# Performance work log

Hardware: AMD Instinct MI355X
Metric: run time of the kernel (lower is better)

## Reference

```python
import jax, jax.numpy as jnp
import numpy as np

D_IN = 4096
D_OUT = 4096
TOKENS = 8192


def setup_inputs() -> dict:
    key = jax.random.key(0)
    k_x, k_w = jax.random.split(key)
    x = jax.random.normal(k_x, (TOKENS, D_IN), dtype=jnp.float32)
    # int8 weight buffer (stored as int32 for jax friendliness; values in [-128,127))
    weight_i8 = jax.random.randint(k_w, (D_OUT, D_IN), -128, 127, dtype=jnp.int32)
    return {
        "x": x,
        "weight_i8": weight_i8,
        "weight_scale": jnp.array([0.01], dtype=jnp.float32),
        "weight_zero_point": jnp.zeros((1,), dtype=jnp.int32),
        "bias": jnp.zeros((D_OUT,), dtype=jnp.float32),
        "output_scale": jnp.array([0.5], dtype=jnp.float32),
        "output_zero_point": jnp.full((1,), 128, dtype=jnp.int32),
    }


def reference(x, weight_i8, weight_scale, weight_zero_point, bias,
              output_scale, output_zero_point):
    # NOTE: the torch module also computes torch.quantize_per_tensor(x, ...)
    # whose result is unused (dead code); it does not affect the output and
    # is omitted here.
    # Dequantize int8 weight: (w_int - zp) * scale  -> [D_OUT, D_IN] fp32
    w = (weight_i8.astype(jnp.float32)
         - weight_zero_point.astype(jnp.float32)) * weight_scale
    # Standard fp32 linear: [T, D_IN] @ [D_IN, D_OUT] + bias
    out = jnp.einsum("ti,oi->to", x, w) + bias
    # quantize_per_tensor(out, output_scale, output_zp, quint8).dequantize():
    # q = clamp(round(out/scale) + zp, 0, 255); deq = (q - zp) * scale
    zp = output_zero_point.astype(jnp.float32)
    q = jnp.clip(jnp.round(out / output_scale) + zp, 0.0, 255.0)
    return (q - zp) * output_scale
```

## Files before the change

kernel.cpp:

```cpp
#include <hip/hip_runtime.h>

#define TOKENS 8192
#define D_IN   4096
#define D_OUT  4096

typedef _Float16 f16;
typedef __attribute__((ext_vector_type(8))) _Float16 half8;
typedef __attribute__((ext_vector_type(4))) float    f32x4;
typedef __attribute__((address_space(3))) char       lds_char;


__global__ void cvt_x_kernel(const float* __restrict__ x, f16* __restrict__ xh) {
    size_t i = ((size_t)blockIdx.x * blockDim.x + threadIdx.x) * 4;
    float4 v = *reinterpret_cast<const float4*>(x + i);
    union { f16 h[4]; uint2 u; } p;
    p.h[0] = (f16)v.x; p.h[1] = (f16)v.y; p.h[2] = (f16)v.z; p.h[3] = (f16)v.w;
    *reinterpret_cast<uint2*>(xh + i) = p.u;
}

__global__ void cvt_w_kernel(const int* __restrict__ w, f16* __restrict__ wh,
                             const float* __restrict__ scale_p,
                             const int* __restrict__ zp_p) {
    size_t i = ((size_t)blockIdx.x * blockDim.x + threadIdx.x) * 4;
    float s = scale_p[0];
    float z = (float)zp_p[0];
    int4 v = *reinterpret_cast<const int4*>(w + i);
    union { f16 h[4]; uint2 u; } p;
    p.h[0] = (f16)(((float)v.x - z) * s);
    p.h[1] = (f16)(((float)v.y - z) * s);
    p.h[2] = (f16)(((float)v.z - z) * s);
    p.h[3] = (f16)(((float)v.w - z) * s);
    *reinterpret_cast<uint2*>(wh + i) = p.u;
}


#define BM 256
#define BN 256
#define BK 64
#define NT (D_IN / BK)
#define LDS_BUF   65536
#define LDS_B_OFF 32768

__device__ __forceinline__ void stage16(const f16* g, lds_char* l) {
    __builtin_amdgcn_global_load_lds(
        (const __attribute__((address_space(1))) void*)g,
        (__attribute__((address_space(3))) void*)l, 16, 0, 0);
}

#define LDS_LOAD8(p) (*(const __attribute__((address_space(3))) half8*)(p))

#define LOAD_A(QM)                                                          \
    do { _Pragma("unroll")                                                  \
        for (int fm = 0; fm < 4; ++fm) {                                    \
            int rr = wr * 128 + (QM) * 64 + fm * 16 + lr;                   \
            _Pragma("unroll")                                               \
            for (int ks = 0; ks < 2; ++ks)                                  \
                a[fm][ks] = LDS_LOAD8(bufA + rr * 128 +                     \
                                      ((cb0 + ks * 64) ^ swzr));            \
        } } while (0)

#define LOAD_B(QN, BV)                                                     \
    do { _Pragma("unroll")                                                  \
        for (int fn = 0; fn < 2; ++fn) {                                    \
            int rr = wc * 64 + (QN) * 32 + fn * 16 + lr;                    \
            _Pragma("unroll")                                               \
            for (int ks = 0; ks < 2; ++ks)                                  \
                BV[fn][ks] = LDS_LOAD8(bufB + rr * 128 +                    \
                                       ((cb0 + ks * 64) ^ swzr));           \
        } } while (0)

#define MFMA_QUAD(QM, QN, BV)                                               \
    do { _Pragma("unroll")                                                  \
        for (int fm = 0; fm < 4; ++fm) {                                    \
            _Pragma("unroll")                                               \
            for (int fn = 0; fn < 2; ++fn) {                                \
                _Pragma("unroll")                                           \
                for (int ks = 0; ks < 2; ++ks)                              \
                    acc[(QM)*4+fm][(QN)*2+fn] =                             \
                        __builtin_amdgcn_mfma_f32_16x16x32_f16(             \
                            a[fm][ks], BV[fn][ks],                          \
                            acc[(QM)*4+fm][(QN)*2+fn], 0, 0, 0);            \
            }                                                               \
        } } while (0)

#define FENCE()    asm volatile("" ::: "memory")
#define BAR()      __builtin_amdgcn_s_barrier()
#define VMCNT(N)   asm volatile("s_waitcnt vmcnt(" #N ")" ::: "memory")
#define PRIO(x)    __builtin_amdgcn_s_setprio(x)

__global__ __launch_bounds__(512, 2)
void gemm8p(const f16* __restrict__ A, const f16* __restrict__ B,
            const float* __restrict__ bias,
            const float* __restrict__ oscale_p, const int* __restrict__ ozp_p,
            float* __restrict__ C)
{
    __shared__ __align__(1024) char smem_[2 * LDS_BUF];
    lds_char* smem = (lds_char*)smem_;
    constexpr int K = D_IN, N = D_OUT;

    int nwg = gridDim.x;
    int cpx = nwg >> 3;
    int bid = blockIdx.x;
    int swz = (bid & 7) * cpx + (bid >> 3);
    int ntn = N / BN;
    int m0 = (swz / ntn) * BM;
    int n0 = (swz % ntn) * BN;

    int tid = threadIdx.x;
    int l   = tid & 63;
    int wv  = tid >> 6;
    int wr  = wv >> 2;
    int wc  = wv & 3;

    int srow = wv * 8 + (l >> 3);
    int scol = ((l & 7) ^ (l >> 3)) * 8;
    const f16* gA = A + (size_t)(m0 + srow) * K + scol;
    const f16* gB = B + (size_t)(n0 + srow) * K + scol;
    lds_char* dstbase = smem + wv * 1024 + l * 16;

    int lr   = l & 15;
    int swzr = (l & 7) << 4;
    int cb0  = (l >> 4) * 16;

    f32x4 acc[8][4] = {};

    #pragma unroll
    for (int q = 0; q < 4; ++q) stage16(gA + (size_t)q * 64 * K, dstbase + q * 8192);
    #pragma unroll
    for (int q = 0; q < 4; ++q) stage16(gB + (size_t)q * 64 * K, dstbase + LDS_B_OFF + q * 8192);
    VMCNT(0);
    BAR();

    half8 a[4][2], b0v[2][2], b1v[2][2];

    for (int t = 0; t < NT - 1; ++t) {
        const lds_char* bufA = smem + (t & 1) * LDS_BUF;
        const lds_char* bufB = bufA + LDS_B_OFF;
        lds_char* dst = dstbase + ((t + 1) & 1) * LDS_BUF;
        const f16* nA = gA + (size_t)(t + 1) * BK;
        const f16* nB = gB + (size_t)(t + 1) * BK;

        LOAD_A(0);
        LOAD_B(0, b0v);
        stage16(nB,                      dst + LDS_B_OFF);
        stage16(nB + (size_t)64 * K,     dst + LDS_B_OFF + 8192);
        BAR();
        PRIO(1); MFMA_QUAD(0, 0, b0v); PRIO(0);

        LOAD_B(1, b1v);
        stage16(nB + (size_t)128 * K,    dst + LDS_B_OFF + 2 * 8192);
        stage16(nB + (size_t)192 * K,    dst + LDS_B_OFF + 3 * 8192);
        BAR();
        PRIO(1); MFMA_QUAD(0, 1, b1v); PRIO(0);

        VMCNT(4);
        BAR();
        LOAD_A(1);
        stage16(nA,                      dst);
        stage16(nA + (size_t)128 * K,    dst + 2 * 8192);
        BAR();
        PRIO(1); MFMA_QUAD(1, 1, b1v); PRIO(0);

        FENCE();
        stage16(nA + (size_t)64 * K,     dst + 8192);
        stage16(nA + (size_t)192 * K,    dst + 3 * 8192);
        BAR();
        PRIO(1); MFMA_QUAD(1, 0, b0v); PRIO(0);

        VMCNT(2);
        BAR();
    }

    {
        const int t = NT - 1;
        const lds_char* bufA = smem + (t & 1) * LDS_BUF;
        const lds_char* bufB = bufA + LDS_B_OFF;

        VMCNT(0);
        BAR();

        LOAD_A(0);
        LOAD_B(0, b0v);
        LOAD_B(1, b1v);
        PRIO(1);
        MFMA_QUAD(0, 0, b0v);
        MFMA_QUAD(0, 1, b1v);
        PRIO(0);
        LOAD_A(1);
        PRIO(1);
        MFMA_QUAD(1, 1, b1v);
        MFMA_QUAD(1, 0, b0v);
        PRIO(0);
    }

    float os  = oscale_p[0];
    float ozp = (float)ozp_p[0];
    float inv = 1.0f / os;
    #pragma unroll
    for (int qm = 0; qm < 2; ++qm) {
        #pragma unroll
        for (int fm = 0; fm < 4; ++fm) {
            int rowb = m0 + wr * 128 + qm * 64 + fm * 16 + (l >> 4) * 4;
            #pragma unroll
            for (int qn = 0; qn < 2; ++qn) {
                #pragma unroll
                for (int fn = 0; fn < 2; ++fn) {
                    int col = n0 + wc * 64 + qn * 32 + fn * 16 + lr;
                    float bv = bias[col];
                    f32x4 v = acc[qm * 4 + fm][qn * 2 + fn];
                    #pragma unroll
                    for (int j = 0; j < 4; ++j) {
                        float o = v[j] + bv;
                        float q = rintf(o * inv) + ozp;
                        q = fminf(fmaxf(q, 0.0f), 255.0f);
                        C[(size_t)(rowb + j) * N + col] = (q - ozp) * os;
                    }
                }
            }
        }
    }
}


extern "C" void kernel_launch(void* const* d_in, const int* in_sizes, int n_in,
                              void* d_out, int out_size, void* d_ws, size_t ws_size,
                              hipStream_t stream) {
    const float* x      = (const float*)d_in[0];
    const int*   w8     = (const int*)d_in[1];
    const float* wscale = (const float*)d_in[2];
    const int*   wzp    = (const int*)d_in[3];
    const float* bias   = (const float*)d_in[4];
    const float* oscale = (const float*)d_in[5];
    const int*   ozp    = (const int*)d_in[6];
    float* out = (float*)d_out;

    const size_t x_elems = (size_t)TOKENS * D_IN;
    const size_t w_elems = (size_t)D_OUT * D_IN;
    const size_t need = (x_elems + w_elems) * sizeof(f16);
    if (ws_size < need) return;

    f16* xh = (f16*)d_ws;
    f16* wh = xh + x_elems;

    {
        int blocks = (int)(x_elems / 4 / 256);
        cvt_x_kernel<<<blocks, 256, 0, stream>>>(x, xh);
    }
    {
        int blocks = (int)(w_elems / 4 / 256);
        cvt_w_kernel<<<blocks, 256, 0, stream>>>(w8, wh, wscale, wzp);
    }
    {
        int grid = (TOKENS / BM) * (D_OUT / BN);
        gemm8p<<<grid, 512, 0, stream>>>(xh, wh, bias, oscale, ozp, out);
    }
}
```

Baseline: 283.0 us.

## Software-pipeline LDS fragment loads across K iterations and drop intra-tile barriers

Restructures the GEMM main loop so the first A and B quadrant fragments for the next K tile are read from LDS at the end of the current iteration, overlapping LDS reads with MFMA work. It removes several per-quadrant barriers and the s_setprio hints, keeping only the barriers tied to the vmcnt waits. Extra register buffers (a0/a1/b0/b0n/b1) raise VGPR pressure, which could hurt occupancy at the launch bound of two blocks of 512 threads. Fewer barriers also leave less explicit ordering between LDS reads and the asynchronous global-to-LDS writes.

```diff
diff --git a/kernel.cpp b/kernel.cpp
--- a/kernel.cpp
+++ b/kernel.cpp
@@ -49,27 +49,27 @@
 
 #define LDS_LOAD8(p) (*(const __attribute__((address_space(3))) half8*)(p))
 
-#define LOAD_A(QM)                                                          \
+#define LOAD_AQ(DST, BUF, QM)                                               \
     do { _Pragma("unroll")                                                  \
         for (int fm = 0; fm < 4; ++fm) {                                    \
             int rr = wr * 128 + (QM) * 64 + fm * 16 + lr;                   \
             _Pragma("unroll")                                               \
             for (int ks = 0; ks < 2; ++ks)                                  \
-                a[fm][ks] = LDS_LOAD8(bufA + rr * 128 +                     \
-                                      ((cb0 + ks * 64) ^ swzr));            \
+                DST[fm][ks] = LDS_LOAD8((BUF) + rr * 128 +                  \
+                                        ((cb0 + ks * 64) ^ swzr));          \
         } } while (0)
 
-#define LOAD_B(QN, BV)                                                     \
+#define LOAD_BQ(DST, BUF, QN)                                               \
     do { _Pragma("unroll")                                                  \
         for (int fn = 0; fn < 2; ++fn) {                                    \
             int rr = wc * 64 + (QN) * 32 + fn * 16 + lr;                    \
             _Pragma("unroll")                                               \
             for (int ks = 0; ks < 2; ++ks)                                  \
-                BV[fn][ks] = LDS_LOAD8(bufB + rr * 128 +                    \
-                                       ((cb0 + ks * 64) ^ swzr));           \
+                DST[fn][ks] = LDS_LOAD8((BUF) + rr * 128 +                  \
+                                        ((cb0 + ks * 64) ^ swzr));          \
         } } while (0)
 
-#define MFMA_QUAD(QM, QN, BV)                                               \
+#define MFMA_Q(QM, QN, AV, BV)                                              \
     do { _Pragma("unroll")                                                  \
         for (int fm = 0; fm < 4; ++fm) {                                    \
             _Pragma("unroll")                                               \
@@ -78,7 +78,7 @@
                 for (int ks = 0; ks < 2; ++ks)                              \
                     acc[(QM)*4+fm][(QN)*2+fn] =                             \
                         __builtin_amdgcn_mfma_f32_16x16x32_f16(             \
-                            a[fm][ks], BV[fn][ks],                          \
+                            AV[fm][ks], BV[fn][ks],                         \
                             acc[(QM)*4+fm][(QN)*2+fn], 0, 0, 0);            \
             }                                                               \
         } } while (0)
@@ -86,13 +86,12 @@
 #define FENCE()    asm volatile("" ::: "memory")
 #define BAR()      __builtin_amdgcn_s_barrier()
 #define VMCNT(N)   asm volatile("s_waitcnt vmcnt(" #N ")" ::: "memory")
-#define PRIO(x)    __builtin_amdgcn_s_setprio(x)
 
 __global__ __launch_bounds__(512, 2)
-void gemm8p(const f16* __restrict__ A, const f16* __restrict__ B,
-            const float* __restrict__ bias,
-            const float* __restrict__ oscale_p, const int* __restrict__ ozp_p,
-            float* __restrict__ C)
+void gemm_pipe(const f16* __restrict__ A, const f16* __restrict__ B,
+               const float* __restrict__ bias,
+               const float* __restrict__ oscale_p, const int* __restrict__ ozp_p,
+               float* __restrict__ C)
 {
     __shared__ __align__(1024) char smem_[2 * LDS_BUF];
     lds_char* smem = (lds_char*)smem_;
@@ -123,6 +122,7 @@
     int cb0  = (l >> 4) * 16;
 
     f32x4 acc[8][4] = {};
+    half8 a0[4][2], a1[4][2], b0[2][2], b0n[2][2], b1[2][2];
 
     #pragma unroll
     for (int q = 0; q < 4; ++q) stage16(gA + (size_t)q * 64 * K, dstbase + q * 8192);
@@ -130,67 +130,66 @@
     for (int q = 0; q < 4; ++q) stage16(gB + (size_t)q * 64 * K, dstbase + LDS_B_OFF + q * 8192);
     VMCNT(0);
     BAR();
-
-    half8 a[4][2], b0v[2][2], b1v[2][2];
+    {
+        const lds_char* bufA = smem;
+        const lds_char* bufB = smem + LDS_B_OFF;
+        LOAD_AQ(a0, bufA, 0);
+        LOAD_BQ(b0, bufB, 0);
+    }
 
     for (int t = 0; t < NT - 1; ++t) {
-        const lds_char* bufA = smem + (t & 1) * LDS_BUF;
-        const lds_char* bufB = bufA + LDS_B_OFF;
+        const lds_char* bufA  = smem + (t & 1) * LDS_BUF;
+        const lds_char* bufB  = bufA + LDS_B_OFF;
+        const lds_char* bufAn = smem + ((t + 1) & 1) * LDS_BUF;
+        const lds_char* bufBn = bufAn + LDS_B_OFF;
         lds_char* dst = dstbase + ((t + 1) & 1) * LDS_BUF;
         const f16* nA = gA + (size_t)(t + 1) * BK;
         const f16* nB = gB + (size_t)(t + 1) * BK;
 
-        LOAD_A(0);
-        LOAD_B(0, b0v);
+        LOAD_BQ(b1, bufB, 1);
         stage16(nB,                      dst + LDS_B_OFF);
         stage16(nB + (size_t)64 * K,     dst + LDS_B_OFF + 8192);
-        BAR();
-        PRIO(1); MFMA_QUAD(0, 0, b0v); PRIO(0);
-
-        LOAD_B(1, b1v);
         stage16(nB + (size_t)128 * K,    dst + LDS_B_OFF + 2 * 8192);
         stage16(nB + (size_t)192 * K,    dst + LDS_B_OFF + 3 * 8192);
-        BAR();
-        PRIO(1); MFMA_QUAD(0, 1, b1v); PRIO(0);
+        MFMA_Q(0, 0, a0, b0);
+        MFMA_Q(0, 1, a0, b1);
 
         VMCNT(4);
         BAR();
-        LOAD_A(1);
+        LOAD_AQ(a1, bufA, 1);
         stage16(nA,                      dst);
         stage16(nA + (size_t)128 * K,    dst + 2 * 8192);
-        BAR();
-        PRIO(1); MFMA_QUAD(1, 1, b1v); PRIO(0);
-
         FENCE();
         stage16(nA + (size_t)64 * K,     dst + 8192);
         stage16(nA + (size_t)192 * K,    dst + 3 * 8192);
-        BAR();
-        PRIO(1); MFMA_QUAD(1, 0, b0v); PRIO(0);
+        MFMA_Q(1, 1, a1, b1);
 
         VMCNT(2);
         BAR();
-    }
-
-    {
-        const int t = NT - 1;
-        const lds_char* bufA = smem + (t & 1) * LDS_BUF;
+        LOAD_AQ(a0, bufAn, 0);
+        LOAD_BQ(b0n, bufBn, 0);
+        MFMA_Q(1, 0, a1, b0);
+
+        #pragma unroll
+        for (int fn = 0; fn < 2; ++fn)
+            #pragma unroll
+            for (int ks = 0; ks < 2; ++ks)
+                b0[fn][ks] = b0n[fn][ks];
+    }
+
+    {
+        const lds_char* bufA = smem + ((NT - 1) & 1) * LDS_BUF;
         const lds_char* bufB = bufA + LDS_B_OFF;
+
+        LOAD_BQ(b1, bufB, 1);
+        MFMA_Q(0, 0, a0, b0);
+        MFMA_Q(0, 1, a0, b1);
 
         VMCNT(0);
         BAR();
-
-        LOAD_A(0);
-        LOAD_B(0, b0v);
-        LOAD_B(1, b1v);
-        PRIO(1);
-        MFMA_QUAD(0, 0, b0v);
-        MFMA_QUAD(0, 1, b1v);
-        PRIO(0);
-        LOAD_A(1);
-        PRIO(1);
-        MFMA_QUAD(1, 1, b1v);
-        MFMA_QUAD(1, 0, b0v);
-        PRIO(0);
+        LOAD_AQ(a1, bufA, 1);
+        MFMA_Q(1, 1, a1, b1);
+        MFMA_Q(1, 0, a1, b0);
     }
 
     float os  = oscale_p[0];
@@ -252,6 +251,6 @@
     }
     {
         int grid = (TOKENS / BM) * (D_OUT / BN);
-        gemm8p<<<grid, 512, 0, stream>>>(xh, wh, bias, oscale, ozp, out);
-    }
-}
+        gemm_pipe<<<grid, 512, 0, stream>>>(xh, wh, bias, oscale, ozp, out);
+    }
+}
```

New measurement: 283.6 us. About the same (+0.2%).

## Switch GEMM inner tile from 16x16x32 to 32x32x16 MFMA instructions

Applied to the files above, without the earlier changes.

Replaces the 16x16x32 f16 MFMA micro-tiles with 32x32x16 MFMA tiles. The LDS fragment load addressing, the swizzle pattern and the epilogue row/column mapping are rewritten to match, while the staging pipeline stays the same. Larger MFMA tiles reuse each LDS-loaded operand across more output elements, which cuts LDS read traffic and instruction count per FLOP. The cost is a different accumulator layout and a possible change in register pressure or bank conflicts.

```diff
diff --git a/kernel.cpp b/kernel.cpp
--- a/kernel.cpp
+++ b/kernel.cpp
@@ -5,9 +5,9 @@
 #define D_OUT  4096
 
 typedef _Float16 f16;
-typedef __attribute__((ext_vector_type(8))) _Float16 half8;
-typedef __attribute__((ext_vector_type(4))) float    f32x4;
-typedef __attribute__((address_space(3))) char       lds_char;
+typedef __attribute__((ext_vector_type(8)))  _Float16 half8;
+typedef __attribute__((ext_vector_type(16))) float    f32x16;
+typedef __attribute__((address_space(3))) char        lds_char;
 
 
 __global__ void cvt_x_kernel(const float* __restrict__ x, f16* __restrict__ xh) {
@@ -49,39 +49,29 @@
 
 #define LDS_LOAD8(p) (*(const __attribute__((address_space(3))) half8*)(p))
 
-#define LOAD_A(QM)                                                          \
+#define LOAD_AH(QM)                                                         \
     do { _Pragma("unroll")                                                  \
-        for (int fm = 0; fm < 4; ++fm) {                                    \
-            int rr = wr * 128 + (QM) * 64 + fm * 16 + lr;                   \
+        for (int mh = 0; mh < 2; ++mh)                                      \
             _Pragma("unroll")                                               \
-            for (int ks = 0; ks < 2; ++ks)                                  \
-                a[fm][ks] = LDS_LOAD8(bufA + rr * 128 +                     \
-                                      ((cb0 + ks * 64) ^ swzr));            \
-        } } while (0)
-
-#define LOAD_B(QN, BV)                                                     \
+            for (int ks = 0; ks < 4; ++ks)                                  \
+                a[mh][ks] = LDS_LOAD8(pAk[ks] + ((QM)*2 + mh) * 4096);      \
+    } while (0)
+
+#define LOAD_BH(BV, QN)                                                     \
     do { _Pragma("unroll")                                                  \
-        for (int fn = 0; fn < 2; ++fn) {                                    \
-            int rr = wc * 64 + (QN) * 32 + fn * 16 + lr;                    \
+        for (int ks = 0; ks < 4; ++ks)                                      \
+            BV[ks] = LDS_LOAD8(pBk[ks] + (QN) * 4096);                      \
+    } while (0)
+
+#define MFMA_Q(QM, QN, BV)                                                  \
+    do { _Pragma("unroll")                                                  \
+        for (int mh = 0; mh < 2; ++mh)                                      \
             _Pragma("unroll")                                               \
-            for (int ks = 0; ks < 2; ++ks)                                  \
-                BV[fn][ks] = LDS_LOAD8(bufB + rr * 128 +                    \
-                                       ((cb0 + ks * 64) ^ swzr));           \
-        } } while (0)
-
-#define MFMA_QUAD(QM, QN, BV)                                               \
-    do { _Pragma("unroll")                                                  \
-        for (int fm = 0; fm < 4; ++fm) {                                    \
-            _Pragma("unroll")                                               \
-            for (int fn = 0; fn < 2; ++fn) {                                \
-                _Pragma("unroll")                                           \
-                for (int ks = 0; ks < 2; ++ks)                              \
-                    acc[(QM)*4+fm][(QN)*2+fn] =                             \
-                        __builtin_amdgcn_mfma_f32_16x16x32_f16(             \
-                            a[fm][ks], BV[fn][ks],                          \
-                            acc[(QM)*4+fm][(QN)*2+fn], 0, 0, 0);            \
-            }                                                               \
-        } } while (0)
+            for (int ks = 0; ks < 4; ++ks)                                  \
+                acc[(QM)*2 + mh][QN] =                                      \
+                    __builtin_amdgcn_mfma_f32_32x32x16_f16(                 \
+                        a[mh][ks], BV[ks], acc[(QM)*2 + mh][QN], 0, 0, 0);  \
+    } while (0)
 
 #define FENCE()    asm volatile("" ::: "memory")
 #define BAR()      __builtin_amdgcn_s_barrier()
@@ -89,7 +79,7 @@
 #define PRIO(x)    __builtin_amdgcn_s_setprio(x)
 
 __global__ __launch_bounds__(512, 2)
-void gemm8p(const f16* __restrict__ A, const f16* __restrict__ B,
+void gemm32(const f16* __restrict__ A, const f16* __restrict__ B,
             const float* __restrict__ bias,
             const float* __restrict__ oscale_p, const int* __restrict__ ozp_p,
             float* __restrict__ C)
@@ -118,11 +108,13 @@
     const f16* gB = B + (size_t)(n0 + srow) * K + scol;
     lds_char* dstbase = smem + wv * 1024 + l * 16;
 
-    int lr   = l & 15;
-    int swzr = (l & 7) << 4;
-    int cb0  = (l >> 4) * 16;
-
-    f32x4 acc[8][4] = {};
+    int lrow = l & 31;
+    int c00  = ((l >> 5) * 16) ^ ((l & 7) << 4);
+    int arow = (wr * 128 + lrow) * 128;
+    int brow = LDS_B_OFF + (wc * 64 + lrow) * 128;
+
+    f32x16 acc[4][2] = {};
+    half8 a[2][4], b0v[4], b1v[4];
 
     #pragma unroll
     for (int q = 0; q < 4; ++q) stage16(gA + (size_t)q * 64 * K, dstbase + q * 8192);
@@ -131,65 +123,75 @@
     VMCNT(0);
     BAR();
 
-    half8 a[4][2], b0v[2][2], b1v[2][2];
-
     for (int t = 0; t < NT - 1; ++t) {
-        const lds_char* bufA = smem + (t & 1) * LDS_BUF;
-        const lds_char* bufB = bufA + LDS_B_OFF;
+        const lds_char* buf = smem + (t & 1) * LDS_BUF;
         lds_char* dst = dstbase + ((t + 1) & 1) * LDS_BUF;
         const f16* nA = gA + (size_t)(t + 1) * BK;
         const f16* nB = gB + (size_t)(t + 1) * BK;
 
-        LOAD_A(0);
-        LOAD_B(0, b0v);
+        const lds_char* pAk[4];
+        const lds_char* pBk[4];
+        #pragma unroll
+        for (int ks = 0; ks < 4; ++ks) {
+            pAk[ks] = buf + arow + (c00 ^ (ks << 5));
+            pBk[ks] = buf + brow + (c00 ^ (ks << 5));
+        }
+
+        LOAD_AH(0);
+        LOAD_BH(b0v, 0);
         stage16(nB,                      dst + LDS_B_OFF);
         stage16(nB + (size_t)64 * K,     dst + LDS_B_OFF + 8192);
         BAR();
-        PRIO(1); MFMA_QUAD(0, 0, b0v); PRIO(0);
-
-        LOAD_B(1, b1v);
+        PRIO(1); MFMA_Q(0, 0, b0v); PRIO(0);
+
+        LOAD_BH(b1v, 1);
         stage16(nB + (size_t)128 * K,    dst + LDS_B_OFF + 2 * 8192);
         stage16(nB + (size_t)192 * K,    dst + LDS_B_OFF + 3 * 8192);
         BAR();
-        PRIO(1); MFMA_QUAD(0, 1, b1v); PRIO(0);
+        PRIO(1); MFMA_Q(0, 1, b1v); PRIO(0);
 
         VMCNT(4);
         BAR();
-        LOAD_A(1);
+        LOAD_AH(1);
         stage16(nA,                      dst);
         stage16(nA + (size_t)128 * K,    dst + 2 * 8192);
         BAR();
-        PRIO(1); MFMA_QUAD(1, 1, b1v); PRIO(0);
+        PRIO(1); MFMA_Q(1, 1, b1v); PRIO(0);
 
         FENCE();
         stage16(nA + (size_t)64 * K,     dst + 8192);
         stage16(nA + (size_t)192 * K,    dst + 3 * 8192);
         BAR();
-        PRIO(1); MFMA_QUAD(1, 0, b0v); PRIO(0);
+        PRIO(1); MFMA_Q(1, 0, b0v); PRIO(0);
 
         VMCNT(2);
         BAR();
     }
 
     {
-        const int t = NT - 1;
-        const lds_char* bufA = smem + (t & 1) * LDS_BUF;
-        const lds_char* bufB = bufA + LDS_B_OFF;
+        const lds_char* buf = smem + ((NT - 1) & 1) * LDS_BUF;
+        const lds_char* pAk[4];
+        const lds_char* pBk[4];
+        #pragma unroll
+        for (int ks = 0; ks < 4; ++ks) {
+            pAk[ks] = buf + arow + (c00 ^ (ks << 5));
+            pBk[ks] = buf + brow + (c00 ^ (ks << 5));
+        }
 
         VMCNT(0);
         BAR();
 
-        LOAD_A(0);
-        LOAD_B(0, b0v);
-        LOAD_B(1, b1v);
+        LOAD_AH(0);
+        LOAD_BH(b0v, 0);
+        LOAD_BH(b1v, 1);
         PRIO(1);
-        MFMA_QUAD(0, 0, b0v);
-        MFMA_QUAD(0, 1, b1v);
+        MFMA_Q(0, 0, b0v);
+        MFMA_Q(0, 1, b1v);
         PRIO(0);
-        LOAD_A(1);
+        LOAD_AH(1);
         PRIO(1);
-        MFMA_QUAD(1, 1, b1v);
-        MFMA_QUAD(1, 0, b0v);
+        MFMA_Q(1, 1, b1v);
+        MFMA_Q(1, 0, b0v);
         PRIO(0);
     }
 
@@ -197,25 +199,20 @@
     float ozp = (float)ozp_p[0];
     float inv = 1.0f / os;
     #pragma unroll
-    for (int qm = 0; qm < 2; ++qm) {
+    for (int mt = 0; mt < 4; ++mt) {
+        int rowb = m0 + wr * 128 + mt * 32 + 4 * (l >> 5);
         #pragma unroll
-        for (int fm = 0; fm < 4; ++fm) {
-            int rowb = m0 + wr * 128 + qm * 64 + fm * 16 + (l >> 4) * 4;
+        for (int nt = 0; nt < 2; ++nt) {
+            int col = n0 + wc * 64 + nt * 32 + (l & 31);
+            float bv = bias[col];
+            f32x16 v = acc[mt][nt];
             #pragma unroll
-            for (int qn = 0; qn < 2; ++qn) {
-                #pragma unroll
-                for (int fn = 0; fn < 2; ++fn) {
-                    int col = n0 + wc * 64 + qn * 32 + fn * 16 + lr;
-                    float bv = bias[col];
-                    f32x4 v = acc[qm * 4 + fm][qn * 2 + fn];
-                    #pragma unroll
-                    for (int j = 0; j < 4; ++j) {
-                        float o = v[j] + bv;
-                        float q = rintf(o * inv) + ozp;
-                        q = fminf(fmaxf(q, 0.0f), 255.0f);
-                        C[(size_t)(rowb + j) * N + col] = (q - ozp) * os;
-                    }
-                }
+            for (int r = 0; r < 16; ++r) {
+                int row = rowb + (r & 3) + 8 * (r >> 2);
+                float o = v[r] + bv;
+                float q = rintf(o * inv) + ozp;
+                q = fminf(fmaxf(q, 0.0f), 255.0f);
+                C[(size_t)row * N + col] = (q - ozp) * os;
             }
         }
     }
@@ -252,6 +249,6 @@
     }
     {
         int grid = (TOKENS / BM) * (D_OUT / BN);
-        gemm8p<<<grid, 512, 0, stream>>>(xh, wh, bias, oscale, ozp, out);
-    }
-}
+        gemm32<<<grid, 512, 0, stream>>>(xh, wh, bias, oscale, ozp, out);
+    }
+}
```

After: 313.0 us. +10.6%, slower.
